# Kernel tuning notes

Measured on AMD Instinct MI355X. Metric: run time of the kernel, lower is better.

The kernel has to match this reference:

```python
import jax, jax.numpy as jnp
import numpy as np

N = 50000        # nodes
E = 600000       # directed edges (before self-loops)
B = 128          # graphs in the batch
D = 128          # in = hidden = out channels (residual requires equality)
HEADS = 4
DH = D // HEADS
L_CONV = 3       # num_layers - 1 hidden convs + 1 out conv = 3 GATconv layers
NEG_SLOPE = 0.2


def setup_inputs() -> dict:
    key = jax.random.key(0)
    ks = jax.random.split(key, 10)
    x = jnp.zeros((N,), dtype=jnp.int64)  # Embedding(1, D) -> all indices are 0
    edge_index = jax.random.randint(ks[0], (2, E), 0, N, dtype=jnp.int64)
    ptr = jnp.sort(jax.random.randint(ks[1], (N,), 0, B, dtype=jnp.int64))
    # parameters (xavier-ish scales)
    emb = jax.random.normal(ks[2], (1, D), dtype=jnp.float32)
    lin_w = jax.random.normal(ks[3], (L_CONV, D, D), dtype=jnp.float32) * (1.0 / np.sqrt(D))
    att_src = jax.random.normal(ks[4], (L_CONV, HEADS, DH), dtype=jnp.float32) * (1.0 / np.sqrt(DH))
    att_dst = jax.random.normal(ks[5], (L_CONV, HEADS, DH), dtype=jnp.float32) * (1.0 / np.sqrt(DH))
    mlp_w0 = jax.random.normal(ks[6], (D, D // 2), dtype=jnp.float32) * (1.0 / np.sqrt(D))
    mlp_b0 = jnp.zeros((D // 2,), dtype=jnp.float32)
    mlp_w1 = jax.random.normal(ks[7], (D // 2, 1), dtype=jnp.float32) * (1.0 / np.sqrt(D // 2))
    mlp_b1 = jnp.zeros((1,), dtype=jnp.float32)
    return {"x": x, "edge_index": edge_index, "ptr": ptr, "emb": emb,
            "lin_w": lin_w, "att_src": att_src, "att_dst": att_dst,
            "mlp_w0": mlp_w0, "mlp_b0": mlp_b0, "mlp_w1": mlp_w1, "mlp_b1": mlp_b1}


def gat_conv(h, src, dst, W, a_src, a_dst):
    # h: [N, D]; src/dst: [E'] (self-loops already appended)
    z = (h @ W).reshape(N, HEADS, DH)                       # [N, H, dh]
    a_s = jnp.einsum('nhd,hd->nh', z, a_src)                # [N, H]
    a_d = jnp.einsum('nhd,hd->nh', z, a_dst)
    alpha = jax.nn.leaky_relu(a_s[src] + a_d[dst], NEG_SLOPE)  # [E', H]
    # segment softmax over destination nodes
    amax = jax.ops.segment_max(alpha, dst, num_segments=N)  # every node has a self-loop
    ex = jnp.exp(alpha - amax[dst])
    den = jax.ops.segment_sum(ex, dst, num_segments=N)
    e_ij = ex / den[dst]                                    # [E', H]
    msg = z[src] * (e_ij[:, :, None] + 1.0)                 # f_additive=True
    out = jax.ops.segment_sum(msg, dst, num_segments=N)     # [N, H, dh]
    return out.reshape(N, D)


def reference(x, edge_index, ptr, emb, lin_w, att_src, att_dst, mlp_w0, mlp_b0, mlp_w1, mlp_b1):
    # add self-loops once (each GATconv adds them to the same edge_index)
    loops = jnp.arange(N, dtype=edge_index.dtype)
    src = jnp.concatenate([edge_index[0], loops])
    dst = jnp.concatenate([edge_index[1], loops])
    h = emb[x]                                              # [N, D] (all rows identical)
    for l in range(L_CONV):
        h = jax.nn.elu(gat_conv(h, src, dst, lin_w[l], att_src[l], att_dst[l])) + h
    # scatter_mean graph readout
    sums = jax.ops.segment_sum(h, ptr, num_segments=B)      # [B, D]
    cnt = jax.ops.segment_sum(jnp.ones((N, 1), h.dtype), ptr, num_segments=B)
    g = sums / jnp.maximum(cnt, 1.0)
    g = jax.nn.relu(g)
    # MLPReadout(D, 1, L=1)
    y = jax.nn.relu(g @ mlp_w0 + mlp_b0)
    y = y @ mlp_w1 + mlp_b1                                 # [B, 1]
    return y
```

## Files before the change

kernel.cpp:

```cpp
#include <hip/hip_runtime.h>
#include <math.h>

#define DIM 128
#define HEADS 4
#define NEG 0.2f
#define ELLW 64

typedef unsigned short u16;
typedef unsigned int u32;
typedef short v8s __attribute__((ext_vector_type(8)));
typedef float v4f __attribute__((ext_vector_type(4)));

static __device__ __forceinline__ float lrelu(float x) { return x >= 0.f ? x : NEG * x; }
static __device__ __forceinline__ u16 f2bf(float f) {
    union { float f; u32 u; } v; v.f = f;
    u32 r = v.u + 0x7fffu + ((v.u >> 16) & 1u);
    return (u16)(r >> 16);
}
static __device__ __forceinline__ float bf2f(u16 b) {
    union { u32 u; float f; } v; v.u = ((u32)b) << 16;
    return v.f;
}
static __device__ __forceinline__ void splitbf(float x, u16& hi, u16& lo) {
    hi = f2bf(x);
    lo = f2bf(x - bf2f(hi));
}

__global__ void k_scatter_prep(const int* __restrict__ ei, int* __restrict__ cnt,
                               int* __restrict__ ell,
                               const float* __restrict__ lin_w, const float* __restrict__ att_s,
                               const float* __restrict__ att_d, u16* __restrict__ WTh,
                               u16* __restrict__ WTl, float* __restrict__ wv,
                               const float* __restrict__ emb, float* __restrict__ z0v,
                               int E, int CB) {
    int b = blockIdx.x;
    if (b < CB) {
        int i = (b * blockDim.x + threadIdx.x) * 2;
        if (i + 1 < E) {
            int2 s2 = *(const int2*)(ei + i);
            int2 d2 = *(const int2*)(ei + E + i);
            int p0 = atomicAdd(&cnt[d2.x], 1);
            int p1 = atomicAdd(&cnt[d2.y], 1);
            if (p0 < ELLW) ell[(size_t)d2.x * ELLW + p0] = s2.x;
            if (p1 < ELLW) ell[(size_t)d2.y * ELLW + p1] = s2.y;
        } else if (i < E) {
            int s = ei[i], d = ei[E + i];
            int p = atomicAdd(&cnt[d], 1);
            if (p < ELLW) ell[(size_t)d * ELLW + p] = s;
        }
    } else if (b < CB + 2) {
        int l = b - CB;
        const float* W = lin_w + (size_t)(l + 1) * DIM * DIM;
        for (int i = threadIdx.x; i < DIM * DIM; i += blockDim.x) {
            int k = i >> 7, n = i & 127;
            u16 hi, lo;
            splitbf(W[k * DIM + n], hi, lo);
            WTh[(size_t)l * DIM * DIM + n * DIM + k] = hi;
            WTl[(size_t)l * DIM * DIM + n * DIM + k] = lo;
        }
        for (int i = threadIdx.x; i < DIM * 8; i += blockDim.x) {
            int c = i >> 3, j = i & 7;
            int hh = j & 3;
            const float* att = (j < 4) ? att_s : att_d;
            float s = 0.f;
            for (int d = 0; d < 32; d++)
                s += W[c * DIM + hh * 32 + d] * att[(size_t)(l + 1) * HEADS * 32 + hh * 32 + d];
            wv[(size_t)l * DIM * 8 + c * 8 + j] = s;
        }
    } else {
        int c = threadIdx.x;
        if (c < DIM) {
            float s = 0.f;
            for (int k = 0; k < DIM; k++) s += emb[k] * lin_w[k * DIM + c];
            z0v[c] = s;
        }
    }
}

__global__ __launch_bounds__(256) void k_hinit(const float* __restrict__ emb,
                                               const float* __restrict__ z0,
                                               const int* __restrict__ cnt,
                                               const float* __restrict__ wv,
                                               u16* __restrict__ hb, u16* __restrict__ hl,
                                               float* __restrict__ a_s, float* __restrict__ a_d,
                                               int N) {
    int tid = threadIdx.x;
    int g = tid & 15;
    int n = blockIdx.x * 16 + (tid >> 4);
    if (n >= N) return;
    float degt = (float)(cnt[n] + 1);
    int c0 = 8 * g;
    float4 za = *(const float4*)(z0 + c0);
    float4 zbv = *(const float4*)(z0 + c0 + 4);
    float4 ea = *(const float4*)(emb + c0);
    float4 eb = *(const float4*)(emb + c0 + 4);
    float zr[8] = {za.x, za.y, za.z, za.w, zbv.x, zbv.y, zbv.z, zbv.w};
    float er[8] = {ea.x, ea.y, ea.z, ea.w, eb.x, eb.y, eb.z, eb.w};
    float out[8];
    #pragma unroll
    for (int c = 0; c < 8; c++) {
        float o = zr[c] * (1.f + degt);
        float e = o > 0.f ? o : (__expf(o) - 1.f);
        out[c] = e + er[c];
    }
    size_t base = (size_t)n * DIM + c0;
    u16 hi[8], lo[8];
    #pragma unroll
    for (int c = 0; c < 8; c++) splitbf(out[c], hi[c], lo[c]);
    uint4 hv, lv;
    hv.x = (u32)hi[0] | ((u32)hi[1] << 16); hv.y = (u32)hi[2] | ((u32)hi[3] << 16);
    hv.z = (u32)hi[4] | ((u32)hi[5] << 16); hv.w = (u32)hi[6] | ((u32)hi[7] << 16);
    lv.x = (u32)lo[0] | ((u32)lo[1] << 16); lv.y = (u32)lo[2] | ((u32)lo[3] << 16);
    lv.z = (u32)lo[4] | ((u32)lo[5] << 16); lv.w = (u32)lo[6] | ((u32)lo[7] << 16);
    *(uint4*)(hb + base) = hv;
    *(uint4*)(hl + base) = lv;
    float p[8] = {};
    #pragma unroll
    for (int c = 0; c < 8; c++) {
        const float* w = wv + (c0 + c) * 8;
        #pragma unroll
        for (int j = 0; j < 8; j++) p[j] += out[c] * w[j];
    }
    #pragma unroll
    for (int off = 1; off < 16; off <<= 1)
        #pragma unroll
        for (int j = 0; j < 8; j++) p[j] += __shfl_xor(p[j], off);
    if (g == 0) {
        #pragma unroll
        for (int j = 0; j < 4; j++) {
            a_s[(size_t)n * HEADS + j] = p[j];
            a_d[(size_t)n * HEADS + j] = p[4 + j];
        }
    }
}

#define LDK 136

__global__ __launch_bounds__(256) void k_gemm(const u16* __restrict__ hbg,
                                              const u16* __restrict__ hlg,
                                              const u16* __restrict__ WTh,
                                              const u16* __restrict__ WTl,
                                              u16* __restrict__ z, int N) {
    __shared__ u16 Bh[64 * LDK];
    __shared__ u16 Bl[64 * LDK];
    int tid = threadIdx.x;
    int wave = tid >> 6, lane = tid & 63;
    int fr = lane & 15, quad = lane >> 4;
    int row0 = blockIdx.x * 64, col0 = blockIdx.y * 64;
    for (int i = tid; i < 64 * 16; i += 256) {
        int r = i >> 4, seg = i & 15;
        *(uint4*)(Bh + r * LDK + seg * 8) = *(const uint4*)(WTh + (size_t)(col0 + r) * DIM + seg * 8);
        *(uint4*)(Bl + r * LDK + seg * 8) = *(const uint4*)(WTl + (size_t)(col0 + r) * DIM + seg * 8);
    }
    int arow = row0 + wave * 16 + fr;
    v8s ah[4], al[4];
    v8s zero8 = {0, 0, 0, 0, 0, 0, 0, 0};
    if (arow < N) {
        #pragma unroll
        for (int ks = 0; ks < 4; ks++) {
            ah[ks] = *(const v8s*)(hbg + (size_t)arow * DIM + ks * 32 + quad * 8);
            al[ks] = *(const v8s*)(hlg + (size_t)arow * DIM + ks * 32 + quad * 8);
        }
    } else {
        #pragma unroll
        for (int ks = 0; ks < 4; ks++) { ah[ks] = zero8; al[ks] = zero8; }
    }
    __syncthreads();
    v4f acc[4] = {};
    #pragma unroll
    for (int ks = 0; ks < 4; ks++) {
        #pragma unroll
        for (int nn = 0; nn < 4; nn++) {
            v8s bh = *(const v8s*)(Bh + (nn * 16 + fr) * LDK + ks * 32 + quad * 8);
            v8s bl = *(const v8s*)(Bl + (nn * 16 + fr) * LDK + ks * 32 + quad * 8);
            acc[nn] = __builtin_amdgcn_mfma_f32_16x16x32_bf16(ah[ks], bh, acc[nn], 0, 0, 0);
            acc[nn] = __builtin_amdgcn_mfma_f32_16x16x32_bf16(ah[ks], bl, acc[nn], 0, 0, 0);
            acc[nn] = __builtin_amdgcn_mfma_f32_16x16x32_bf16(al[ks], bh, acc[nn], 0, 0, 0);
        }
    }
    int rbase = row0 + wave * 16 + quad * 4;
    #pragma unroll
    for (int nn = 0; nn < 4; nn++) {
        int colg = col0 + nn * 16 + fr;
        #pragma unroll
        for (int r = 0; r < 4; r++) {
            int gr = rbase + r;
            if (gr < N) z[(size_t)gr * DIM + colg] = f2bf(acc[nn][r]);
        }
    }
}

static __device__ __forceinline__ void accw2(uint4 zv, float ex, float msk,
                                             float* acc1, float* acc2) {
    u32 w[4] = {zv.x, zv.y, zv.z, zv.w};
    #pragma unroll
    for (int q = 0; q < 4; q++) {
        union { u32 u; float f; } lo, hi;
        lo.u = w[q] << 16;
        hi.u = w[q] & 0xffff0000u;
        acc1[2 * q] += lo.f * ex;      acc2[2 * q] += lo.f * msk;
        acc1[2 * q + 1] += hi.f * ex;  acc2[2 * q + 1] += hi.f * msk;
    }
}

__global__ __launch_bounds__(256) void k_aggr(const u16* __restrict__ zb,
                                              const float* __restrict__ a_s,
                                              const float* __restrict__ a_d,
                                              const int* __restrict__ cnt,
                                              const int* __restrict__ ell,
                                              u16* __restrict__ hb, u16* __restrict__ hl,
                                              const float* __restrict__ wvn,
                                              float* __restrict__ as_out,
                                              float* __restrict__ ad_out,
                                              float* __restrict__ gbuf,
                                              const int* __restrict__ ptr, int N) {
    __shared__ float arr[16][132];
    __shared__ int gids[16];
    int tid = threadIdx.x;
    int g = tid & 15, node = tid >> 4;
    int n0 = blockIdx.x * 16;
    int n = n0 + node;
    bool active = n < N;
    int hh = g >> 2;
    float out[8];
    if (active) {
        int m = cnt[n];
        if (m > ELLW) m = ELLW;
        const int* row = ell + (size_t)n * ELLW;
        float ad = a_d[(size_t)n * HEADS + hh];
        float mx = lrelu(a_s[(size_t)n * HEADS + hh] + ad);
        float den = 1.f;
        float acc1[8] = {}, acc2[8] = {};
        {
            uint4 zv = *(const uint4*)(zb + (size_t)n * DIM + 8 * g);
            accw2(zv, 1.f, 1.f, acc1, acc2);
        }
        int groups = (m + 3) >> 2;
        for (int t = 0; t < groups; t += 2) {
            int jb = t * 4;
            int4 sa = *(const int4*)(row + jb);
            int4 sb = *(const int4*)(row + jb + 4);
            int idx[8];
            idx[0] = (jb + 0 < m) ? sa.x : n;
            idx[1] = (jb + 1 < m) ? sa.y : n;
            idx[2] = (jb + 2 < m) ? sa.z : n;
            idx[3] = (jb + 3 < m) ? sa.w : n;
            idx[4] = (jb + 4 < m) ? sb.x : n;
            idx[5] = (jb + 5 < m) ? sb.y : n;
            idx[6] = (jb + 6 < m) ? sb.z : n;
            idx[7] = (jb + 7 < m) ? sb.w : n;
            float q[8];
            #pragma unroll
            for (int k = 0; k < 8; k++) q[k] = a_s[(size_t)idx[k] * HEADS + hh];
            uint4 zv[8];
            #pragma unroll
            for (int k = 0; k < 8; k++) zv[k] = *(const uint4*)(zb + (size_t)idx[k] * DIM + 8 * g);
            float l[8];
            #pragma unroll
            for (int k = 0; k < 8; k++)
                l[k] = (jb + k < m) ? lrelu(q[k] + ad) : -1e30f;
            float m8 = l[0];
            #pragma unroll
            for (int k = 1; k < 8; k++) m8 = fmaxf(m8, l[k]);
            if (m8 > mx) {
                float sc = __expf(mx - m8);
                den *= sc;
                #pragma unroll
                for (int c = 0; c < 8; c++) acc1[c] *= sc;
                mx = m8;
            }
            #pragma unroll
            for (int k = 0; k < 8; k++) {
                float ex = __expf(l[k] - mx);
                float msk = (jb + k < m) ? 1.f : 0.f;
                den += ex;
                accw2(zv[k], ex, msk, acc1, acc2);
            }
        }
        float inv = 1.f / den;
        size_t base = (size_t)n * DIM + 8 * g;
        uint4 hbi = *(const uint4*)(hb + base);
        uint4 hli = *(const uint4*)(hl + base);
        u32 hw[4] = {hbi.x, hbi.y, hbi.z, hbi.w};
        u32 lw[4] = {hli.x, hli.y, hli.z, hli.w};
        #pragma unroll
        for (int q2 = 0; q2 < 4; q2++) {
            float h0 = bf2f((u16)(hw[q2] & 0xffff)) + bf2f((u16)(lw[q2] & 0xffff));
            float h1 = bf2f((u16)(hw[q2] >> 16)) + bf2f((u16)(lw[q2] >> 16));
            float o0 = acc1[2 * q2] * inv + acc2[2 * q2];
            float o1 = acc1[2 * q2 + 1] * inv + acc2[2 * q2 + 1];
            float e0 = o0 > 0.f ? o0 : (__expf(o0) - 1.f);
            float e1 = o1 > 0.f ? o1 : (__expf(o1) - 1.f);
            out[2 * q2] = h0 + e0;
            out[2 * q2 + 1] = h1 + e1;
        }
    } else {
        #pragma unroll
        for (int c = 0; c < 8; c++) out[c] = 0.f;
    }

    if (!gbuf) {
        if (active) {
            size_t base = (size_t)n * DIM + 8 * g;
            u16 chi[8], clo[8];
            #pragma unroll
            for (int c = 0; c < 8; c++) splitbf(out[c], chi[c], clo[c]);
            uint4 hv, lv;
            hv.x = (u32)chi[0] | ((u32)chi[1] << 16); hv.y = (u32)chi[2] | ((u32)chi[3] << 16);
            hv.z = (u32)chi[4] | ((u32)chi[5] << 16); hv.w = (u32)chi[6] | ((u32)chi[7] << 16);
            lv.x = (u32)clo[0] | ((u32)clo[1] << 16); lv.y = (u32)clo[2] | ((u32)clo[3] << 16);
            lv.z = (u32)clo[4] | ((u32)clo[5] << 16); lv.w = (u32)clo[6] | ((u32)clo[7] << 16);
            *(uint4*)(hb + base) = hv;
            *(uint4*)(hl + base) = lv;
            if (wvn) {
                float p[8] = {};
                int c0 = 8 * g;
                #pragma unroll
                for (int c = 0; c < 8; c++) {
                    const float* w = wvn + (c0 + c) * 8;
                    #pragma unroll
                    for (int jj = 0; jj < 8; jj++) p[jj] += out[c] * w[jj];
                }
                #pragma unroll
                for (int off = 1; off < 16; off <<= 1)
                    #pragma unroll
                    for (int jj = 0; jj < 8; jj++) p[jj] += __shfl_xor(p[jj], off);
                if (g == 0) {
                    #pragma unroll
                    for (int jj = 0; jj < 4; jj++) {
                        as_out[(size_t)n * HEADS + jj] = p[jj];
                        ad_out[(size_t)n * HEADS + jj] = p[4 + jj];
                    }
                }
            }
        }
    } else {
        *(float4*)&arr[node][8 * g] = make_float4(out[0], out[1], out[2], out[3]);
        *(float4*)&arr[node][8 * g + 4] = make_float4(out[4], out[5], out[6], out[7]);
        if (tid < 16) gids[tid] = (n0 + tid < N) ? ptr[n0 + tid] : -1;
        __syncthreads();
        if (tid < 128) {
            int c = tid;
            float acc2 = 0.f;
            int cur = -1;
            #pragma unroll
            for (int i = 0; i < 16; i++) {
                int gid = gids[i];
                if (gid != cur) {
                    if (cur >= 0) atomicAdd(&gbuf[(size_t)cur * DIM + c], acc2);
                    cur = gid;
                    acc2 = 0.f;
                }
                if (gid >= 0) acc2 += arr[i][c];
            }
            if (cur >= 0) atomicAdd(&gbuf[(size_t)cur * DIM + c], acc2);
        }
    }
}

__global__ __launch_bounds__(128) void k_red2(const float* __restrict__ g,
                                              const int* __restrict__ ptr,
                                              const float* __restrict__ w0,
                                              const float* __restrict__ b0,
                                              const float* __restrict__ w1,
                                              const float* __restrict__ b1,
                                              float* __restrict__ y, int N) {
    __shared__ float gsh[DIM];
    int b = blockIdx.x;
    int tid = threadIdx.x;
    int lo = 0, hi = N;
    while (lo < hi) { int m = (lo + hi) >> 1; if (ptr[m] < b) lo = m + 1; else hi = m; }
    int start = lo;
    hi = N;
    while (lo < hi) { int m = (lo + hi) >> 1; if (ptr[m] < b + 1) lo = m + 1; else hi = m; }
    int end = lo;
    float cnt = (float)(end - start);
    float gv = g[(size_t)b * DIM + tid] / fmaxf(cnt, 1.f);
    gsh[tid] = fmaxf(gv, 0.f);
    __syncthreads();
    if (tid < 64) {
        float hj = b0[tid];
        for (int k = 0; k < DIM; k++) hj += gsh[k] * w0[k * 64 + tid];
        hj = fmaxf(hj, 0.f);
        float p = hj * w1[tid];
        #pragma unroll
        for (int off = 32; off > 0; off >>= 1) p += __shfl_down(p, off);
        if (tid == 0) y[b] = p + b1[0];
    }
}

extern "C" void kernel_launch(void* const* d_in, const int* in_sizes, int n_in,
                              void* d_out, int out_size, void* d_ws, size_t ws_size,
                              hipStream_t stream) {
    const int* ei = (const int*)d_in[1];
    const int* ptr = (const int*)d_in[2];
    const float* emb = (const float*)d_in[3];
    const float* lin_w = (const float*)d_in[4];
    const float* att_s = (const float*)d_in[5];
    const float* att_d = (const float*)d_in[6];
    const float* w0 = (const float*)d_in[7];
    const float* b0 = (const float*)d_in[8];
    const float* w1 = (const float*)d_in[9];
    const float* b1 = (const float*)d_in[10];
    float* y = (float*)d_out;

    const int N = in_sizes[0];
    const int E = in_sizes[1] / 2;
    const int B = out_size;

    char* wp = (char*)d_ws;
    auto alloc = [&](size_t bytes) {
        void* p = (void*)wp;
        wp += (bytes + 255) & ~(size_t)255;
        return p;
    };
    u16* hb = (u16*)alloc((size_t)N * DIM * 2);
    u16* hl = (u16*)alloc((size_t)N * DIM * 2);
    u16* zb = (u16*)alloc((size_t)N * DIM * 2);
    int* ell = (int*)alloc(((size_t)N * ELLW + 8) * 4);
    float* a_s0 = (float*)alloc((size_t)N * HEADS * 4);
    float* a_d0 = (float*)alloc((size_t)N * HEADS * 4);
    float* a_s1 = (float*)alloc((size_t)N * HEADS * 4);
    float* a_d1 = (float*)alloc((size_t)N * HEADS * 4);
    int* cnt = (int*)alloc((size_t)N * 4);
    float* gbuf = (float*)alloc((size_t)B * DIM * 4);
    size_t zspan = (size_t)(wp - (char*)cnt);
    float* z0 = (float*)alloc(DIM * 4);
    u16* WTh = (u16*)alloc((size_t)2 * DIM * DIM * 2);
    u16* WTl = (u16*)alloc((size_t)2 * DIM * DIM * 2);
    float* wv = (float*)alloc((size_t)2 * DIM * 8 * 4);

    hipMemsetAsync(cnt, 0, zspan, stream);

    int CB = ((E + 1) / 2 + 255) / 256;
    k_scatter_prep<<<CB + 3, 256, 0, stream>>>(ei, cnt, ell, lin_w, att_s, att_d,
                                               WTh, WTl, wv, emb, z0, E, CB);
    k_hinit<<<(N + 15) / 16, 256, 0, stream>>>(emb, z0, cnt, wv, hb, hl, a_s0, a_d0, N);

    dim3 ggrid((N + 63) / 64, 2);
    int ablocks = (N + 15) / 16;
    k_gemm<<<ggrid, 256, 0, stream>>>(hb, hl, WTh, WTl, zb, N);
    k_aggr<<<ablocks, 256, 0, stream>>>(zb, a_s0, a_d0, cnt, ell, hb, hl,
                                        wv + (size_t)DIM * 8, a_s1, a_d1,
                                        nullptr, nullptr, N);
    k_gemm<<<ggrid, 256, 0, stream>>>(hb, hl, WTh + (size_t)DIM * DIM,
                                      WTl + (size_t)DIM * DIM, zb, N);
    k_aggr<<<ablocks, 256, 0, stream>>>(zb, a_s1, a_d1, cnt, ell, hb, hl,
                                        nullptr, nullptr, nullptr,
                                        gbuf, ptr, N);

    k_red2<<<B, 128, 0, stream>>>(gbuf, ptr, w0, b0, w1, b1, y, N);
}
```

Baseline: 289.9 us.

## Build ELL adjacency with per-block node partitions and shared-memory atomics

Replaces the global-atomic edge scatter with 64 blocks of 1024 threads. Each block scans the full destination array and keeps only edges whose destination falls in its own node range, counting them with shared-memory atomics. It then writes its counts straight to the global count array, so the large zeroing memset shrinks to the graph readout buffer only. The cost is that every block re-reads all edge destinations, and only 64 blocks work on this stage, which may leave much of the GPU idle.

Result: slower. 392.9 us (+35.5%).

```diff
diff --git a/kernel.cpp b/kernel.cpp
--- a/kernel.cpp
+++ b/kernel.cpp
@@ -5,6 +5,7 @@
 #define HEADS 4
 #define NEG 0.2f
 #define ELLW 64
+#define PBLK 64
 
 typedef unsigned short u16;
 typedef unsigned int u32;
@@ -26,30 +27,51 @@
     lo = f2bf(x - bf2f(hi));
 }
 
-__global__ void k_scatter_prep(const int* __restrict__ ei, int* __restrict__ cnt,
-                               int* __restrict__ ell,
-                               const float* __restrict__ lin_w, const float* __restrict__ att_s,
-                               const float* __restrict__ att_d, u16* __restrict__ WTh,
-                               u16* __restrict__ WTl, float* __restrict__ wv,
-                               const float* __restrict__ emb, float* __restrict__ z0v,
-                               int E, int CB) {
+__global__ __launch_bounds__(1024) void k_build(const int* __restrict__ ei, int* __restrict__ cnt,
+                                                int* __restrict__ ell,
+                                                const float* __restrict__ lin_w,
+                                                const float* __restrict__ att_s,
+                                                const float* __restrict__ att_d,
+                                                u16* __restrict__ WTh, u16* __restrict__ WTl,
+                                                float* __restrict__ wv,
+                                                const float* __restrict__ emb,
+                                                float* __restrict__ z0v,
+                                                int E, int N) {
     int b = blockIdx.x;
-    if (b < CB) {
-        int i = (b * blockDim.x + threadIdx.x) * 2;
-        if (i + 1 < E) {
-            int2 s2 = *(const int2*)(ei + i);
-            int2 d2 = *(const int2*)(ei + E + i);
-            int p0 = atomicAdd(&cnt[d2.x], 1);
-            int p1 = atomicAdd(&cnt[d2.y], 1);
-            if (p0 < ELLW) ell[(size_t)d2.x * ELLW + p0] = s2.x;
-            if (p1 < ELLW) ell[(size_t)d2.y * ELLW + p1] = s2.y;
-        } else if (i < E) {
-            int s = ei[i], d = ei[E + i];
-            int p = atomicAdd(&cnt[d], 1);
-            if (p < ELLW) ell[(size_t)d * ELLW + p] = s;
-        }
-    } else if (b < CB + 2) {
-        int l = b - CB;
+    if (b < PBLK) {
+        __shared__ int lcnt[832];
+        int span = (N + PBLK - 1) / PBLK;
+        int n0 = b * span;
+        int n1 = n0 + span < N ? n0 + span : N;
+        int sp = n1 - n0;
+        for (int i = threadIdx.x; i < sp; i += blockDim.x) lcnt[i] = 0;
+        __syncthreads();
+        const int* dst = ei + E;
+        int i0 = threadIdx.x * 4;
+        int stride = blockDim.x * 4;
+        for (; i0 + 3 < E; i0 += stride) {
+            int4 d4 = *(const int4*)(dst + i0);
+            int dd[4] = {d4.x, d4.y, d4.z, d4.w};
+            #pragma unroll
+            for (int k = 0; k < 4; k++) {
+                int d = dd[k];
+                if (d >= n0 && d < n1) {
+                    int p = atomicAdd(&lcnt[d - n0], 1);
+                    if (p < ELLW) ell[(size_t)d * ELLW + p] = ei[i0 + k];
+                }
+            }
+        }
+        for (; i0 < E; i0++) {
+            int d = dst[i0];
+            if (d >= n0 && d < n1) {
+                int p = atomicAdd(&lcnt[d - n0], 1);
+                if (p < ELLW) ell[(size_t)d * ELLW + p] = ei[i0];
+            }
+        }
+        __syncthreads();
+        for (int i = threadIdx.x; i < sp; i += blockDim.x) cnt[n0 + i] = lcnt[i];
+    } else if (b < PBLK + 2) {
+        int l = b - PBLK;
         const float* W = lin_w + (size_t)(l + 1) * DIM * DIM;
         for (int i = threadIdx.x; i < DIM * DIM; i += blockDim.x) {
             int k = i >> 7, n = i & 127;
@@ -424,17 +446,15 @@
     float* a_d1 = (float*)alloc((size_t)N * HEADS * 4);
     int* cnt = (int*)alloc((size_t)N * 4);
     float* gbuf = (float*)alloc((size_t)B * DIM * 4);
-    size_t zspan = (size_t)(wp - (char*)cnt);
     float* z0 = (float*)alloc(DIM * 4);
     u16* WTh = (u16*)alloc((size_t)2 * DIM * DIM * 2);
     u16* WTl = (u16*)alloc((size_t)2 * DIM * DIM * 2);
     float* wv = (float*)alloc((size_t)2 * DIM * 8 * 4);
 
-    hipMemsetAsync(cnt, 0, zspan, stream);
-
-    int CB = ((E + 1) / 2 + 255) / 256;
-    k_scatter_prep<<<CB + 3, 256, 0, stream>>>(ei, cnt, ell, lin_w, att_s, att_d,
-                                               WTh, WTl, wv, emb, z0, E, CB);
+    hipMemsetAsync(gbuf, 0, (size_t)B * DIM * 4, stream);
+
+    k_build<<<PBLK + 3, 1024, 0, stream>>>(ei, cnt, ell, lin_w, att_s, att_d,
+                                           WTh, WTl, wv, emb, z0, E, N);
     k_hinit<<<(N + 15) / 16, 256, 0, stream>>>(emb, z0, cnt, wv, hb, hl, a_s0, a_d0, N);
 
     dim3 ggrid((N + 63) / 64, 2);
```

## Replace first GATconv layer GEMM with per-degree lookup tables

Applied to the files above, without the earlier changes.

Every node starts from the same embedding, so the layer-0 output and its layer-1 projection depend only on in-degree. The change precomputes h, z = h·W1 and attention logits for each degree value 0..64 in a new table kernel. A new first aggregation kernel then reads those tables instead of running a node-wise init plus a full GEMM and gather over z. This removes one GEMM pass and the dense h/z traffic for that layer. Separately, per-node edge counters are padded to 64-byte stride to reduce atomic contention during ELL construction, at the cost of a larger memset.

Measured after the change: 265.1 us. -8.5%, faster.

```diff
diff --git a/kernel.cpp b/kernel.cpp
--- a/kernel.cpp
+++ b/kernel.cpp
@@ -26,7 +26,7 @@
     lo = f2bf(x - bf2f(hi));
 }
 
-__global__ void k_scatter_prep(const int* __restrict__ ei, int* __restrict__ cnt,
+__global__ void k_scatter_prep(const int* __restrict__ ei, int* __restrict__ cnt16,
                                int* __restrict__ ell,
                                const float* __restrict__ lin_w, const float* __restrict__ att_s,
                                const float* __restrict__ att_d, u16* __restrict__ WTh,
@@ -35,36 +35,31 @@
                                int E, int CB) {
     int b = blockIdx.x;
     if (b < CB) {
-        int i = (b * blockDim.x + threadIdx.x) * 2;
-        if (i + 1 < E) {
-            int2 s2 = *(const int2*)(ei + i);
-            int2 d2 = *(const int2*)(ei + E + i);
-            int p0 = atomicAdd(&cnt[d2.x], 1);
-            int p1 = atomicAdd(&cnt[d2.y], 1);
-            if (p0 < ELLW) ell[(size_t)d2.x * ELLW + p0] = s2.x;
-            if (p1 < ELLW) ell[(size_t)d2.y * ELLW + p1] = s2.y;
-        } else if (i < E) {
+        int i = b * blockDim.x + threadIdx.x;
+        if (i < E) {
             int s = ei[i], d = ei[E + i];
-            int p = atomicAdd(&cnt[d], 1);
+            int p = atomicAdd(&cnt16[(size_t)d * 16], 1);
             if (p < ELLW) ell[(size_t)d * ELLW + p] = s;
         }
-    } else if (b < CB + 2) {
-        int l = b - CB;
-        const float* W = lin_w + (size_t)(l + 1) * DIM * DIM;
+    } else if (b == CB) {
+        const float* W = lin_w + (size_t)2 * DIM * DIM;
         for (int i = threadIdx.x; i < DIM * DIM; i += blockDim.x) {
             int k = i >> 7, n = i & 127;
             u16 hi, lo;
             splitbf(W[k * DIM + n], hi, lo);
-            WTh[(size_t)l * DIM * DIM + n * DIM + k] = hi;
-            WTl[(size_t)l * DIM * DIM + n * DIM + k] = lo;
-        }
-        for (int i = threadIdx.x; i < DIM * 8; i += blockDim.x) {
-            int c = i >> 3, j = i & 7;
+            WTh[n * DIM + k] = hi;
+            WTl[n * DIM + k] = lo;
+        }
+        for (int i = threadIdx.x; i < DIM * 8 * 2; i += blockDim.x) {
+            int l = i / (DIM * 8);
+            int r = i % (DIM * 8);
+            int c = r >> 3, j = r & 7;
             int hh = j & 3;
+            const float* Wl = lin_w + (size_t)(l + 1) * DIM * DIM;
             const float* att = (j < 4) ? att_s : att_d;
             float s = 0.f;
             for (int d = 0; d < 32; d++)
-                s += W[c * DIM + hh * 32 + d] * att[(size_t)(l + 1) * HEADS * 32 + hh * 32 + d];
+                s += Wl[c * DIM + hh * 32 + d] * att[(size_t)(l + 1) * HEADS * 32 + hh * 32 + d];
             wv[(size_t)l * DIM * 8 + c * 8 + j] = s;
         }
     } else {
@@ -77,59 +72,180 @@
     }
 }
 
-__global__ __launch_bounds__(256) void k_hinit(const float* __restrict__ emb,
-                                               const float* __restrict__ z0,
-                                               const int* __restrict__ cnt,
-                                               const float* __restrict__ wv,
+__global__ __launch_bounds__(256) void k_tables(const float* __restrict__ z0,
+                                                const float* __restrict__ emb,
+                                                const float* __restrict__ lin_w,
+                                                const float* __restrict__ wv,
+                                                const int* __restrict__ cnt16,
+                                                int* __restrict__ deg,
+                                                float* __restrict__ htab,
+                                                float* __restrict__ ztab,
+                                                float* __restrict__ atab_s,
+                                                float* __restrict__ atab_d, int N) {
+    int b = blockIdx.x;
+    if (b < 65) {
+        __shared__ float h0sh[DIM];
+        __shared__ float psh[DIM][8];
+        int c = threadIdx.x;
+        int d = b;
+        if (c < DIM) {
+            float degt = (float)(d + 1);
+            float o = z0[c] * (1.f + degt);
+            float e = o > 0.f ? o : (__expf(o) - 1.f);
+            float h0 = e + emb[c];
+            htab[d * DIM + c] = h0;
+            h0sh[c] = h0;
+            const float* w = wv + c * 8;
+            #pragma unroll
+            for (int j = 0; j < 8; j++) psh[c][j] = h0 * w[j];
+        }
+        __syncthreads();
+        if (c < 8) {
+            float s = 0.f;
+            for (int k = 0; k < DIM; k++) s += psh[k][c];
+            if (c < 4) atab_s[d * 4 + c] = s;
+            else       atab_d[d * 4 + (c - 4)] = s;
+        }
+        if (c < DIM) {
+            const float* W1 = lin_w + (size_t)DIM * DIM;
+            float s = 0.f;
+            for (int k = 0; k < DIM; k++) s += h0sh[k] * W1[k * DIM + c];
+            ztab[d * DIM + c] = s;
+        }
+    } else {
+        int n = (b - 65) * 256 + threadIdx.x;
+        if (n < N) deg[n] = cnt16[(size_t)n * 16];
+    }
+}
+
+__global__ __launch_bounds__(256) void k_aggr1(const int* __restrict__ deg,
+                                               const int* __restrict__ ell,
+                                               const float* __restrict__ htab,
+                                               const float* __restrict__ ztab,
+                                               const float* __restrict__ atab_s,
+                                               const float* __restrict__ atab_d,
                                                u16* __restrict__ hb, u16* __restrict__ hl,
-                                               float* __restrict__ a_s, float* __restrict__ a_d,
-                                               int N) {
+                                               const float* __restrict__ wvn,
+                                               float* __restrict__ as_out,
+                                               float* __restrict__ ad_out, int N) {
     int tid = threadIdx.x;
     int g = tid & 15;
     int n = blockIdx.x * 16 + (tid >> 4);
     if (n >= N) return;
-    float degt = (float)(cnt[n] + 1);
+    int hh = g >> 2;
+    int dn = deg[n];
+    int m = dn < ELLW ? dn : ELLW;
+    int tn = dn < 64 ? dn : 64;
+    const int* row = ell + (size_t)n * ELLW;
+    float ad = atab_d[tn * 4 + hh];
+    float mx = lrelu(atab_s[tn * 4 + hh] + ad);
+    float den = 1.f;
+    float acc1[8] = {}, acc2[8] = {};
+    {
+        const float* zr = ztab + tn * DIM + 8 * g;
+        float4 a = *(const float4*)zr, bq = *(const float4*)(zr + 4);
+        float zs[8] = {a.x, a.y, a.z, a.w, bq.x, bq.y, bq.z, bq.w};
+        #pragma unroll
+        for (int c = 0; c < 8; c++) { acc1[c] += zs[c]; acc2[c] += zs[c]; }
+    }
+    int groups = (m + 3) >> 2;
+    for (int t = 0; t < groups; t += 2) {
+        int jb = t * 4;
+        int4 sa = *(const int4*)(row + jb);
+        int4 sb = *(const int4*)(row + jb + 4);
+        int idx[8];
+        idx[0] = (jb + 0 < m) ? sa.x : n;
+        idx[1] = (jb + 1 < m) ? sa.y : n;
+        idx[2] = (jb + 2 < m) ? sa.z : n;
+        idx[3] = (jb + 3 < m) ? sa.w : n;
+        idx[4] = (jb + 4 < m) ? sb.x : n;
+        idx[5] = (jb + 5 < m) ? sb.y : n;
+        idx[6] = (jb + 6 < m) ? sb.z : n;
+        idx[7] = (jb + 7 < m) ? sb.w : n;
+        int ts[8];
+        #pragma unroll
+        for (int k = 0; k < 8; k++) {
+            int ds = deg[idx[k]];
+            ts[k] = ds < 64 ? ds : 64;
+        }
+        float l[8];
+        #pragma unroll
+        for (int k = 0; k < 8; k++)
+            l[k] = (jb + k < m) ? lrelu(atab_s[ts[k] * 4 + hh] + ad) : -1e30f;
+        float m8 = l[0];
+        #pragma unroll
+        for (int k = 1; k < 8; k++) m8 = fmaxf(m8, l[k]);
+        if (m8 > mx) {
+            float sc = __expf(mx - m8);
+            den *= sc;
+            #pragma unroll
+            for (int c = 0; c < 8; c++) acc1[c] *= sc;
+            mx = m8;
+        }
+        #pragma unroll
+        for (int half = 0; half < 2; half++) {
+            float4 za[4], zq[4];
+            #pragma unroll
+            for (int k = 0; k < 4; k++) {
+                const float* zr = ztab + ts[half * 4 + k] * DIM + 8 * g;
+                za[k] = *(const float4*)zr;
+                zq[k] = *(const float4*)(zr + 4);
+            }
+            #pragma unroll
+            for (int k = 0; k < 4; k++) {
+                int kk = half * 4 + k;
+                float ex = __expf(l[kk] - mx);
+                float msk = (jb + kk < m) ? 1.f : 0.f;
+                den += ex;
+                float zs[8] = {za[k].x, za[k].y, za[k].z, za[k].w,
+                               zq[k].x, zq[k].y, zq[k].z, zq[k].w};
+                #pragma unroll
+                for (int c = 0; c < 8; c++) {
+                    acc1[c] += zs[c] * ex;
+                    acc2[c] += zs[c] * msk;
+                }
+            }
+        }
+    }
+    float inv = 1.f / den;
+    const float* hr = htab + tn * DIM + 8 * g;
+    float4 ha = *(const float4*)hr, hq = *(const float4*)(hr + 4);
+    float hv[8] = {ha.x, ha.y, ha.z, ha.w, hq.x, hq.y, hq.z, hq.w};
+    float out[8];
+    #pragma unroll
+    for (int c = 0; c < 8; c++) {
+        float o = acc1[c] * inv + acc2[c];
+        float e = o > 0.f ? o : (__expf(o) - 1.f);
+        out[c] = hv[c] + e;
+    }
+    size_t base = (size_t)n * DIM + 8 * g;
+    u16 chi[8], clo[8];
+    #pragma unroll
+    for (int c = 0; c < 8; c++) splitbf(out[c], chi[c], clo[c]);
+    uint4 hvv, lvv;
+    hvv.x = (u32)chi[0] | ((u32)chi[1] << 16); hvv.y = (u32)chi[2] | ((u32)chi[3] << 16);
+    hvv.z = (u32)chi[4] | ((u32)chi[5] << 16); hvv.w = (u32)chi[6] | ((u32)chi[7] << 16);
+    lvv.x = (u32)clo[0] | ((u32)clo[1] << 16); lvv.y = (u32)clo[2] | ((u32)clo[3] << 16);
+    lvv.z = (u32)clo[4] | ((u32)clo[5] << 16); lvv.w = (u32)clo[6] | ((u32)clo[7] << 16);
+    *(uint4*)(hb + base) = hvv;
+    *(uint4*)(hl + base) = lvv;
+    float p[8] = {};
     int c0 = 8 * g;
-    float4 za = *(const float4*)(z0 + c0);
-    float4 zbv = *(const float4*)(z0 + c0 + 4);
-    float4 ea = *(const float4*)(emb + c0);
-    float4 eb = *(const float4*)(emb + c0 + 4);
-    float zr[8] = {za.x, za.y, za.z, za.w, zbv.x, zbv.y, zbv.z, zbv.w};
-    float er[8] = {ea.x, ea.y, ea.z, ea.w, eb.x, eb.y, eb.z, eb.w};
-    float out[8];
     #pragma unroll
     for (int c = 0; c < 8; c++) {
-        float o = zr[c] * (1.f + degt);
-        float e = o > 0.f ? o : (__expf(o) - 1.f);
-        out[c] = e + er[c];
-    }
-    size_t base = (size_t)n * DIM + c0;
-    u16 hi[8], lo[8];
-    #pragma unroll
-    for (int c = 0; c < 8; c++) splitbf(out[c], hi[c], lo[c]);
-    uint4 hv, lv;
-    hv.x = (u32)hi[0] | ((u32)hi[1] << 16); hv.y = (u32)hi[2] | ((u32)hi[3] << 16);
-    hv.z = (u32)hi[4] | ((u32)hi[5] << 16); hv.w = (u32)hi[6] | ((u32)hi[7] << 16);
-    lv.x = (u32)lo[0] | ((u32)lo[1] << 16); lv.y = (u32)lo[2] | ((u32)lo[3] << 16);
-    lv.z = (u32)lo[4] | ((u32)lo[5] << 16); lv.w = (u32)lo[6] | ((u32)lo[7] << 16);
-    *(uint4*)(hb + base) = hv;
-    *(uint4*)(hl + base) = lv;
-    float p[8] = {};
-    #pragma unroll
-    for (int c = 0; c < 8; c++) {
-        const float* w = wv + (c0 + c) * 8;
-        #pragma unroll
-        for (int j = 0; j < 8; j++) p[j] += out[c] * w[j];
+        const float* w = wvn + (c0 + c) * 8;
+        #pragma unroll
+        for (int jj = 0; jj < 8; jj++) p[jj] += out[c] * w[jj];
     }
     #pragma unroll
     for (int off = 1; off < 16; off <<= 1)
         #pragma unroll
-        for (int j = 0; j < 8; j++) p[j] += __shfl_xor(p[j], off);
+        for (int jj = 0; jj < 8; jj++) p[jj] += __shfl_xor(p[jj], off);
     if (g == 0) {
         #pragma unroll
-        for (int j = 0; j < 4; j++) {
-            a_s[(size_t)n * HEADS + j] = p[j];
-            a_d[(size_t)n * HEADS + j] = p[4 + j];
+        for (int jj = 0; jj < 4; jj++) {
+            as_out[(size_t)n * HEADS + jj] = p[jj];
+            ad_out[(size_t)n * HEADS + jj] = p[4 + jj];
         }
     }
 }
@@ -203,17 +319,15 @@
     }
 }
 
-__global__ __launch_bounds__(256) void k_aggr(const u16* __restrict__ zb,
-                                              const float* __restrict__ a_s,
-                                              const float* __restrict__ a_d,
-                                              const int* __restrict__ cnt,
-                                              const int* __restrict__ ell,
-                                              u16* __restrict__ hb, u16* __restrict__ hl,
-                                              const float* __restrict__ wvn,
-                                              float* __restrict__ as_out,
-                                              float* __restrict__ ad_out,
-                                              float* __restrict__ gbuf,
-                                              const int* __restrict__ ptr, int N) {
+__global__ __launch_bounds__(256) void k_aggr2(const u16* __restrict__ zb,
+                                               const float* __restrict__ a_s,
+                                               const float* __restrict__ a_d,
+                                               const int* __restrict__ deg,
+                                               const int* __restrict__ ell,
+                                               const u16* __restrict__ hb,
+                                               const u16* __restrict__ hl,
+                                               float* __restrict__ gbuf,
+                                               const int* __restrict__ ptr, int N) {
     __shared__ float arr[16][132];
     __shared__ int gids[16];
     int tid = threadIdx.x;
@@ -224,7 +338,7 @@
     int hh = g >> 2;
     float out[8];
     if (active) {
-        int m = cnt[n];
+        int m = deg[n];
         if (m > ELLW) m = ELLW;
         const int* row = ell + (size_t)n * ELLW;
         float ad = a_d[(size_t)n * HEADS + hh];
@@ -298,63 +412,25 @@
         #pragma unroll
         for (int c = 0; c < 8; c++) out[c] = 0.f;
     }
-
-    if (!gbuf) {
-        if (active) {
-            size_t base = (size_t)n * DIM + 8 * g;
-            u16 chi[8], clo[8];
-            #pragma unroll
-            for (int c = 0; c < 8; c++) splitbf(out[c], chi[c], clo[c]);
-            uint4 hv, lv;
-            hv.x = (u32)chi[0] | ((u32)chi[1] << 16); hv.y = (u32)chi[2] | ((u32)chi[3] << 16);
-            hv.z = (u32)chi[4] | ((u32)chi[5] << 16); hv.w = (u32)chi[6] | ((u32)chi[7] << 16);
-            lv.x = (u32)clo[0] | ((u32)clo[1] << 16); lv.y = (u32)clo[2] | ((u32)clo[3] << 16);
-            lv.z = (u32)clo[4] | ((u32)clo[5] << 16); lv.w = (u32)clo[6] | ((u32)clo[7] << 16);
-            *(uint4*)(hb + base) = hv;
-            *(uint4*)(hl + base) = lv;
-            if (wvn) {
-                float p[8] = {};
-                int c0 = 8 * g;
-                #pragma unroll
-                for (int c = 0; c < 8; c++) {
-                    const float* w = wvn + (c0 + c) * 8;
-                    #pragma unroll
-                    for (int jj = 0; jj < 8; jj++) p[jj] += out[c] * w[jj];
-                }
-                #pragma unroll
-                for (int off = 1; off < 16; off <<= 1)
-                    #pragma unroll
-                    for (int jj = 0; jj < 8; jj++) p[jj] += __shfl_xor(p[jj], off);
-                if (g == 0) {
-                    #pragma unroll
-                    for (int jj = 0; jj < 4; jj++) {
-                        as_out[(size_t)n * HEADS + jj] = p[jj];
-                        ad_out[(size_t)n * HEADS + jj] = p[4 + jj];
-                    }
-                }
+    *(float4*)&arr[node][8 * g] = make_float4(out[0], out[1], out[2], out[3]);
+    *(float4*)&arr[node][8 * g + 4] = make_float4(out[4], out[5], out[6], out[7]);
+    if (tid < 16) gids[tid] = (n0 + tid < N) ? ptr[n0 + tid] : -1;
+    __syncthreads();
+    if (tid < 128) {
+        int c = tid;
+        float acc2 = 0.f;
+        int cur = -1;
+        #pragma unroll
+        for (int i = 0; i < 16; i++) {
+            int gid = gids[i];
+            if (gid != cur) {
+                if (cur >= 0) atomicAdd(&gbuf[(size_t)cur * DIM + c], acc2);
+                cur = gid;
+                acc2 = 0.f;
             }
-        }
-    } else {
-        *(float4*)&arr[node][8 * g] = make_float4(out[0], out[1], out[2], out[3]);
-        *(float4*)&arr[node][8 * g + 4] = make_float4(out[4], out[5], out[6], out[7]);
-        if (tid < 16) gids[tid] = (n0 + tid < N) ? ptr[n0 + tid] : -1;
-        __syncthreads();
-        if (tid < 128) {
-            int c = tid;
-            float acc2 = 0.f;
-            int cur = -1;
-            #pragma unroll
-            for (int i = 0; i < 16; i++) {
-                int gid = gids[i];
-                if (gid != cur) {
-                    if (cur >= 0) atomicAdd(&gbuf[(size_t)cur * DIM + c], acc2);
-                    cur = gid;
-                    acc2 = 0.f;
-                }
-                if (gid >= 0) acc2 += arr[i][c];
-            }
-            if (cur >= 0) atomicAdd(&gbuf[(size_t)cur * DIM + c], acc2);
-        }
+            if (gid >= 0) acc2 += arr[i][c];
+        }
+        if (cur >= 0) atomicAdd(&gbuf[(size_t)cur * DIM + c], acc2);
     }
 }
 
@@ -418,36 +494,35 @@
     u16* hl = (u16*)alloc((size_t)N * DIM * 2);
     u16* zb = (u16*)alloc((size_t)N * DIM * 2);
     int* ell = (int*)alloc(((size_t)N * ELLW + 8) * 4);
-    float* a_s0 = (float*)alloc((size_t)N * HEADS * 4);
-    float* a_d0 = (float*)alloc((size_t)N * HEADS * 4);
     float* a_s1 = (float*)alloc((size_t)N * HEADS * 4);
     float* a_d1 = (float*)alloc((size_t)N * HEADS * 4);
-    int* cnt = (int*)alloc((size_t)N * 4);
+    int* deg = (int*)alloc((size_t)N * 4);
+    int* cnt16 = (int*)alloc((size_t)N * 16 * 4);
     float* gbuf = (float*)alloc((size_t)B * DIM * 4);
-    size_t zspan = (size_t)(wp - (char*)cnt);
+    size_t zspan = (size_t)(wp - (char*)cnt16);
     float* z0 = (float*)alloc(DIM * 4);
-    u16* WTh = (u16*)alloc((size_t)2 * DIM * DIM * 2);
-    u16* WTl = (u16*)alloc((size_t)2 * DIM * DIM * 2);
+    u16* WTh = (u16*)alloc((size_t)DIM * DIM * 2);
+    u16* WTl = (u16*)alloc((size_t)DIM * DIM * 2);
     float* wv = (float*)alloc((size_t)2 * DIM * 8 * 4);
-
-    hipMemsetAsync(cnt, 0, zspan, stream);
-
-    int CB = ((E + 1) / 2 + 255) / 256;
-    k_scatter_prep<<<CB + 3, 256, 0, stream>>>(ei, cnt, ell, lin_w, att_s, att_d,
+    float* htab = (float*)alloc((size_t)65 * DIM * 4);
+    float* ztab = (float*)alloc((size_t)65 * DIM * 4);
+    float* atab_s = (float*)alloc((size_t)65 * 4 * 4);
+    float* atab_d = (float*)alloc((size_t)65 * 4 * 4);
+
+    hipMemsetAsync(cnt16, 0, zspan, stream);
+
+    int CB = (E + 255) / 256;
+    k_scatter_prep<<<CB + 2, 256, 0, stream>>>(ei, cnt16, ell, lin_w, att_s, att_d,
                                                WTh, WTl, wv, emb, z0, E, CB);
-    k_hinit<<<(N + 15) / 16, 256, 0, stream>>>(emb, z0, cnt, wv, hb, hl, a_s0, a_d0, N);
-
+    int TB = 65 + (N + 255) / 256;
+    k_tables<<<TB, 256, 0, stream>>>(z0, emb, lin_w, wv, cnt16, deg,
+                                     htab, ztab, atab_s, atab_d, N);
+    int ablocks = (N + 15) / 16;
+    k_aggr1<<<ablocks, 256, 0, stream>>>(deg, ell, htab, ztab, atab_s, atab_d,
+                                         hb, hl, wv + (size_t)DIM * 8, a_s1, a_d1, N);
     dim3 ggrid((N + 63) / 64, 2);
-    int ablocks = (N + 15) / 16;
     k_gemm<<<ggrid, 256, 0, stream>>>(hb, hl, WTh, WTl, zb, N);
-    k_aggr<<<ablocks, 256, 0, stream>>>(zb, a_s0, a_d0, cnt, ell, hb, hl,
-                                        wv + (size_t)DIM * 8, a_s1, a_d1,
-                                        nullptr, nullptr, N);
-    k_gemm<<<ggrid, 256, 0, stream>>>(hb, hl, WTh + (size_t)DIM * DIM,
-                                      WTl + (size_t)DIM * DIM, zb, N);
-    k_aggr<<<ablocks, 256, 0, stream>>>(zb, a_s1, a_d1, cnt, ell, hb, hl,
-                                        nullptr, nullptr, nullptr,
-                                        gbuf, ptr, N);
+    k_aggr2<<<ablocks, 256, 0, stream>>>(zb, a_s1, a_d1, deg, ell, hb, hl, gbuf, ptr, N);
 
     k_red2<<<B, 128, 0, stream>>>(gbuf, ptr, w0, b0, w1, b1, y, N);
 }
```
